# Performance work log

Measured on AMD Instinct MI355X. Metric: run time of the kernel, lower is better.

## Reference

```python
import jax, jax.numpy as jnp
import numpy as np

N = 50000
NUM_GRAPHS = 64
EPS = 1e-16  # PyG softmax denominator epsilon


def _gat_conv(x, src, dst, W, a_src, a_dst, b, heads, out_ch):
    n = x.shape[0]
    h = (x @ W).reshape(n, heads, out_ch)                    # [N,H,C]
    al_s = jnp.einsum('nhc,hc->nh', h, a_src)                # [N,H]
    al_d = jnp.einsum('nhc,hc->nh', h, a_dst)                # [N,H]
    e = jax.nn.leaky_relu(al_s[src] + al_d[dst], 0.2)        # [E,H]
    emax = jax.ops.segment_max(e, dst, num_segments=n)       # [N,H]
    ee = jnp.exp(e - emax[dst])
    den = jax.ops.segment_sum(ee, dst, num_segments=n)       # [N,H]
    alpha = ee / (den[dst] + EPS)                            # [E,H]
    msg = h[src] * alpha[:, :, None]                         # [E,H,C]
    out = jax.ops.segment_sum(msg, dst, num_segments=n)      # [N,H,C]
    return out.reshape(n, heads * out_ch) + b


def setup_inputs() -> dict:
    key = jax.random.key(0)
    ks = jax.random.split(key, 16)
    E = 250000
    x = jax.random.normal(ks[0], (N, 11), dtype=jnp.float32)
    edge_index = jax.random.randint(ks[1], (2, E), 0, N, dtype=jnp.int64)
    batch = jnp.sort(jax.random.randint(ks[2], (N,), 0, NUM_GRAPHS, dtype=jnp.int64))
    def glorot(k, shape):
        fan = shape[0] + shape[-1]
        return jax.random.uniform(k, shape, jnp.float32, -1.0, 1.0) * np.sqrt(6.0 / fan)
    return {
        'x': x, 'edge_index': edge_index, 'batch': batch,
        'W1': glorot(ks[3], (11, 8 * 128)),
        'a1s': glorot(ks[4], (8, 128)), 'a1d': glorot(ks[5], (8, 128)),
        'b1': jnp.zeros((8 * 128,), jnp.float32),
        'W2': glorot(ks[6], (1024, 8 * 64)),
        'a2s': glorot(ks[7], (8, 64)), 'a2d': glorot(ks[8], (8, 64)),
        'b2': jnp.zeros((8 * 64,), jnp.float32),
        'W3': glorot(ks[9], (512, 4 * 32)),
        'a3s': glorot(ks[10], (4, 32)), 'a3d': glorot(ks[11], (4, 32)),
        'b3': jnp.zeros((4 * 32,), jnp.float32),
        'Wout': glorot(ks[12], (128, 1)),
        'bout': jnp.zeros((1,), jnp.float32),
    }


def reference(x, edge_index, batch, W1, a1s, a1d, b1, W2, a2s, a2d, b2,
              W3, a3s, a3d, b3, Wout, bout):
    n = x.shape[0]
    # GATConv adds self-loops by default
    loop = jnp.arange(n, dtype=edge_index.dtype)
    src = jnp.concatenate([edge_index[0], loop])
    dst = jnp.concatenate([edge_index[1], loop])
    h = jax.nn.leaky_relu(_gat_conv(x, src, dst, W1, a1s, a1d, b1, 8, 128), 0.01)
    h = jax.nn.leaky_relu(_gat_conv(h, src, dst, W2, a2s, a2d, b2, 8, 64), 0.01)
    h = jax.nn.leaky_relu(_gat_conv(h, src, dst, W3, a3s, a3d, b3, 4, 32), 0.01)
    # global mean pool over graphs
    sums = jax.ops.segment_sum(h, batch, num_segments=NUM_GRAPHS)      # [G,128]
    cnt = jax.ops.segment_sum(jnp.ones((n,), h.dtype), batch, num_segments=NUM_GRAPHS)
    pooled = sums / jnp.maximum(cnt, 1.0)[:, None]
    return pooled @ Wout + bout                                        # [G,1]
```

## Files before the change

kernel.cpp:

```cpp
#include <hip/hip_runtime.h>

#define EPS 1e-16f

typedef __attribute__((ext_vector_type(8))) short short8;
typedef __attribute__((ext_vector_type(4))) float f32x4;

__device__ __forceinline__ float b2f(unsigned short u) {
    return __uint_as_float(((unsigned)u) << 16);
}
__device__ __forceinline__ unsigned short f2b(float f) {
    unsigned u = __float_as_uint(f);
    u += 0x7fffu + ((u >> 16) & 1u);
    return (unsigned short)(u >> 16);
}

typedef __attribute__((address_space(3))) void lds_vp;
typedef __attribute__((address_space(1))) const void glb_vp;
__device__ __forceinline__ void load_lds16(const unsigned short* g,
                                           unsigned short* l) {
    __builtin_amdgcn_global_load_lds((glb_vp*)g, (lds_vp*)l, 16, 0, 0);
}

__global__ void init_deg_kernel(int* deg, int N) {
    int i = blockIdx.x * blockDim.x + threadIdx.x;
    if (i < N) deg[i] = 1;
}

__global__ void hist_kernel(const int* __restrict__ ei, int E, int N, int* deg) {
    int e = blockIdx.x * blockDim.x + threadIdx.x;
    if (e < E) {
        int d = ei[E + e];
        if ((unsigned)d < (unsigned)N) atomicAdd(&deg[d], 1);
    }
}

__global__ void scan_block_kernel(const int* __restrict__ deg,
                                  int* __restrict__ rowst,
                                  int* __restrict__ bsum, int N) {
    __shared__ int s[256];
    int t = threadIdx.x, b = blockIdx.x;
    int i = b * 256 + t;
    s[t] = (i < N) ? deg[i] : 0;
    __syncthreads();
    for (int o = 1; o < 256; o <<= 1) {
        int a = (t >= o) ? s[t - o] : 0;
        __syncthreads();
        s[t] += a;
        __syncthreads();
    }
    if (i < N) rowst[i + 1] = s[t];
    if (t == 255) bsum[b] = s[255];
}

__global__ void scan_top_kernel(const int* __restrict__ bsum,
                                int* __restrict__ boff, int NB) {
    __shared__ int psum[65];
    int t = threadIdx.x;
    int chunk = (NB + 63) / 64;
    int lo = t * chunk, hi = lo + chunk;
    if (lo > NB) lo = NB;
    if (hi > NB) hi = NB;
    int s = 0;
    for (int i = lo; i < hi; i++) s += bsum[i];
    psum[t + 1] = s;
    __syncthreads();
    if (t == 0) {
        psum[0] = 0;
        for (int i = 1; i <= 64; i++) psum[i] += psum[i - 1];
    }
    __syncthreads();
    int run = psum[t];
    for (int i = lo; i < hi; i++) {
        boff[i] = run;
        run += bsum[i];
    }
}

__global__ void scan_finish_kernel(int* __restrict__ rowst,
                                   const int* __restrict__ boff,
                                   const int* __restrict__ deg,
                                   int* __restrict__ srcs,
                                   int* __restrict__ cursor, int N) {
    int i = blockIdx.x * 256 + threadIdx.x;
    if (i == 0) rowst[0] = 0;
    if (i < N) {
        int incl = rowst[i + 1] + boff[blockIdx.x];
        rowst[i + 1] = incl;
        int st = incl - deg[i];
        srcs[st] = i;
        cursor[i] = st + 1;
    }
}

__global__ void scatter_kernel(const int* __restrict__ ei, int E, int N,
                               int* cursor, int* srcs) {
    int e = blockIdx.x * blockDim.x + threadIdx.x;
    if (e < E) {
        int d = ei[E + e];
        if ((unsigned)d < (unsigned)N) {
            int p = atomicAdd(&cursor[d], 1);
            int s = ei[e];
            if ((unsigned)s >= (unsigned)N) s = d;
            srcs[p] = s;
        }
    }
}

__global__ void wprep_kernel(const float* __restrict__ W1,
                             const float* __restrict__ W2,
                             const float* __restrict__ W3,
                             unsigned short* __restrict__ wt2,
                             unsigned short* __restrict__ wt3,
                             unsigned short* __restrict__ w1sk) {
    int i = blockIdx.x * blockDim.x + threadIdx.x;
    if (i < 1024 * 512) {
        int k = i / 512, n = i % 512;
        wt2[(size_t)n * 1024 + k] = f2b(W2[i]);
    } else if (i < 1024 * 512 + 512 * 128) {
        int j = i - 1024 * 512;
        int k = j / 128, n = j % 128;
        wt3[(size_t)n * 512 + k] = f2b(W3[j]);
    } else if (i < 1024 * 512 + 512 * 128 + 8 * 128 * 32) {
        int q = i - (1024 * 512 + 512 * 128);
        int h = q >> 12, rem = q & 4095;
        int c = rem >> 5, kk = rem & 31;
        int off = (h == 7) ? 16 : 0;
        float v = 0.f;
        int k = kk - off;
        if (k >= 0 && k < 11) v = W1[k * 1024 + h * 128 + c];
        w1sk[q] = f2b(v);
    }
}

__global__ void al1_kernel(const float* __restrict__ x,
                           const float* __restrict__ W1,
                           const float* __restrict__ a1s,
                           const float* __restrict__ a1d,
                           float* __restrict__ als, float* __restrict__ ald,
                           int N) {
    __shared__ float was[128], wad[128];
    int t = threadIdx.x;
    if (t < 88) {
        int h = t / 11, k = t % 11;
        float s = 0.f, d = 0.f;
        for (int c = 0; c < 128; c++) {
            float w = W1[k * 1024 + h * 128 + c];
            s += w * a1s[h * 128 + c];
            d += w * a1d[h * 128 + c];
        }
        was[h * 16 + k] = s;
        wad[h * 16 + k] = d;
    }
    __syncthreads();
    int i = blockIdx.x * 256 + t;
    if (i >= N * 8) return;
    int n = i >> 3, h = i & 7;
    float s = 0.f, d = 0.f;
#pragma unroll
    for (int k = 0; k < 11; k++) {
        float xv = x[n * 11 + k];
        s += xv * was[h * 16 + k];
        d += xv * wad[h * 16 + k];
    }
    als[i] = s;
    ald[i] = d;
}

__global__ void aggx_kernel(const float* __restrict__ x,
                            const float* __restrict__ als,
                            const float* __restrict__ ald,
                            const int* __restrict__ rowst,
                            const int* __restrict__ srcs,
                            unsigned short* __restrict__ A2, int N) {
    int n = blockIdx.x;
    int t = threadIdx.x;
    int h = t >> 4, k = t & 15;
    int start = rowst[n], end = rowst[n + 1];
    float aldn = ald[n * 8 + h];
    float m = -1e30f;
    for (int idx = start + k; idx < end; idx += 16) {
        float v = als[srcs[idx] * 8 + h] + aldn;
        v = v > 0.f ? v : 0.2f * v;
        m = fmaxf(m, v);
    }
#pragma unroll
    for (int o = 1; o < 16; o <<= 1) m = fmaxf(m, __shfl_xor(m, o));
    float den = 0.f;
    for (int idx = start + k; idx < end; idx += 16) {
        float v = als[srcs[idx] * 8 + h] + aldn;
        v = v > 0.f ? v : 0.2f * v;
        den += expf(v - m);
    }
#pragma unroll
    for (int o = 1; o < 16; o <<= 1) den += __shfl_xor(den, o);
    float dinv = 1.0f / (den + EPS);

    float acc = 0.f;
    const int CH = 4;
    for (int idx = start; idx < end; idx += CH) {
        int mc = end - idx;
        if (mc > CH) mc = CH;
        int ss[CH];
        float lv[CH], xv[CH];
#pragma unroll
        for (int j = 0; j < CH; j++)
            if (j < mc) ss[j] = srcs[idx + j];
#pragma unroll
        for (int j = 0; j < CH; j++)
            if (j < mc) lv[j] = als[ss[j] * 8 + h];
#pragma unroll
        for (int j = 0; j < CH; j++)
            if (j < mc) xv[j] = (k < 11) ? x[ss[j] * 11 + k] : 0.f;
#pragma unroll
        for (int j = 0; j < CH; j++)
            if (j < mc) {
                float v = lv[j] + aldn;
                v = v > 0.f ? v : 0.2f * v;
                acc += expf(v - m) * dinv * xv[j];
            }
    }
    A2[(size_t)n * 128 + t] = f2b(acc);
}

template <bool EPI, int HB, int CC, bool SK>
__global__ __launch_bounds__(256) void gemm_mfma(
    const unsigned short* __restrict__ A, const unsigned short* __restrict__ Bt,
    unsigned short* __restrict__ C, const float* __restrict__ bias,
    const float* __restrict__ a_s, const float* __restrict__ a_d,
    float* __restrict__ als, float* __restrict__ ald, int H, int M, int N,
    int K, int lda) {
    int NX = gridDim.x;
    int bid = blockIdx.y * NX + blockIdx.x;
    int win = bid & (8 * NX - 1);
    int mg = bid / (8 * NX);
    int m_t = mg * 8 + (win & 7);
    int n_t = win >> 3;
    int bm = m_t * 128, bn = n_t * 128;
    if (bm >= M) return;

    union SMem {
        struct {
            unsigned short As[2][128 * 32];
            unsigned short Bs[2][128 * 32];
        } k;
        unsigned short Ct[128 * 132];
    };
    __shared__ __align__(16) SMem sm;
    auto& As = sm.k.As;
    auto& Bs = sm.k.Bs;
    auto& Ct = sm.Ct;

    int t = threadIdx.x;
    int w = t >> 6, lane = t & 63;
    int quad = lane >> 4, l16 = lane & 15;
    int wr = (w >> 1) * 64, wc = (w & 1) * 64;

    int kofs = 0;
    const unsigned short* Bb = Bt;
    if (SK) {
        kofs = n_t * 16;
        if (kofs > lda - 32) kofs = lda - 32;
        Bb = Bt + (size_t)n_t * 128 * 32;
    }

    int c0 = w * 128 + lane;
    int c1 = c0 + 64;
    int r0 = c0 >> 2, p0 = c0 & 3;
    int r1 = c1 >> 2, p1 = c1 & 3;
    int j0 = (p0 - (r0 >> 1)) & 3;
    int j1 = (p1 - (r1 >> 1)) & 3;
    int ga0 = bm + r0;
    if (ga0 >= M) ga0 = M - 1;
    int ga1 = bm + r1;
    if (ga1 >= M) ga1 = M - 1;
    const unsigned short* Ag0 = A + (size_t)ga0 * lda + kofs + j0 * 8;
    const unsigned short* Ag1 = A + (size_t)ga1 * lda + kofs + j1 * 8;
    size_t br0 = SK ? (size_t)r0 : (size_t)(bn + r0);
    size_t br1 = SK ? (size_t)r1 : (size_t)(bn + r1);
    const unsigned short* Bg0 = Bb + br0 * K + j0 * 8;
    const unsigned short* Bg1 = Bb + br1 * K + j1 * 8;

    auto stage = [&](int st, int k0) {
        load_lds16(Ag0 + k0, &As[st][(w * 128) * 8]);
        load_lds16(Ag1 + k0, &As[st][(w * 128 + 64) * 8]);
        load_lds16(Bg0 + k0, &Bs[st][(w * 128) * 8]);
        load_lds16(Bg1 + k0, &Bs[st][(w * 128 + 64) * 8]);
    };

    int aoff[4], boff4[4];
#pragma unroll
    for (int i = 0; i < 4; i++) {
        int ra = wr + i * 16 + l16;
        aoff[i] = ra * 32 + (((quad + (ra >> 1)) & 3) * 8);
        int rb = wc + i * 16 + l16;
        boff4[i] = rb * 32 + (((quad + (rb >> 1)) & 3) * 8);
    }

    f32x4 acc[4][4] = {};
    stage(0, 0);
    int st = 0;
    for (int k0 = 0; k0 < K; k0 += 32, st ^= 1) {
        __syncthreads();
        if (k0 + 32 < K) stage(st ^ 1, k0 + 32);
        short8 a[4], b[4];
#pragma unroll
        for (int mi = 0; mi < 4; mi++) a[mi] = *(const short8*)&As[st][aoff[mi]];
#pragma unroll
        for (int ni = 0; ni < 4; ni++) b[ni] = *(const short8*)&Bs[st][boff4[ni]];
#pragma unroll
        for (int mi = 0; mi < 4; mi++)
#pragma unroll
            for (int ni = 0; ni < 4; ni++)
                acc[mi][ni] = __builtin_amdgcn_mfma_f32_16x16x32_bf16(
                    a[mi], b[ni], acc[mi][ni], 0, 0, 0);
    }
    __syncthreads();

#pragma unroll
    for (int mi = 0; mi < 4; mi++) {
#pragma unroll
        for (int r = 0; r < 4; r++) {
            int rl = wr + mi * 16 + quad * 4 + r;
#pragma unroll
            for (int ni = 0; ni < 4; ni++) {
                int cl = wc + ni * 16 + l16;
                float v = acc[mi][ni][r];
                if (EPI) {
                    v += bias[bn + cl];
                    v = v > 0.f ? v : 0.01f * v;
                }
                Ct[rl * 132 + cl] = f2b(v);
            }
        }
    }
    __syncthreads();
#pragma unroll
    for (int p = 0; p < 16; p++) {
        int q = p * 256 + t;
        int row = q >> 5, c8 = q & 31;
        if (bm + row < M) {
            uint2 v = *(const uint2*)&Ct[row * 132 + c8 * 4];
            *(uint2*)&C[(size_t)(bm + row) * N + bn + c8 * 4] = v;
        }
    }
    if (HB > 0) {
        for (int pi = t; pi < 128 * HB; pi += 256) {
            int row = pi / HB, hl = pi % HB;
            if (bm + row >= M) continue;
            int hg = bn / CC + hl;
            const unsigned short* rp = &Ct[row * 132 + hl * CC];
            const float* asp = a_s + hg * CC;
            const float* adp = a_d + hg * CC;
            float s = 0.f, d = 0.f;
#pragma unroll
            for (int c = 0; c < CC; c++) {
                float v = b2f(rp[c]);
                s += v * asp[c];
                d += v * adp[c];
            }
            als[(size_t)(bm + row) * H + hg] = s;
            ald[(size_t)(bm + row) * H + hg] = d;
        }
    }
}

template <int H, int C>
__global__ void agg_fused4(const unsigned short* __restrict__ hin,
                           const float* __restrict__ als,
                           const float* __restrict__ ald,
                           const int* __restrict__ rowst,
                           const int* __restrict__ srcs,
                           const float* __restrict__ bias,
                           unsigned short* __restrict__ out, int N) {
    constexpr int HC = H * C;
    constexpr int TPH = C / 4;
    int n = blockIdx.x;
    int t = threadIdx.x;
    int c = t * 4;
    int hh = c / C;
    int li = (c % C) / 4;
    int start = rowst[n], end = rowst[n + 1];
    float aldn = ald[n * H + hh];
    float m = -1e30f;
    for (int idx = start + li; idx < end; idx += TPH) {
        float v = als[srcs[idx] * H + hh] + aldn;
        v = v > 0.f ? v : 0.2f * v;
        m = fmaxf(m, v);
    }
#pragma unroll
    for (int o = 1; o < TPH; o <<= 1) m = fmaxf(m, __shfl_xor(m, o));
    float den = 0.f;
    for (int idx = start + li; idx < end; idx += TPH) {
        float v = als[srcs[idx] * H + hh] + aldn;
        v = v > 0.f ? v : 0.2f * v;
        den += expf(v - m);
    }
#pragma unroll
    for (int o = 1; o < TPH; o <<= 1) den += __shfl_xor(den, o);
    float dinv = 1.0f / (den + EPS);

    float a0 = 0.f, a1 = 0.f, a2 = 0.f, a3 = 0.f;
    const int CH = 4;
    for (int idx = start; idx < end; idx += CH) {
        int mc = end - idx;
        if (mc > CH) mc = CH;
        int ss[CH];
        float lv[CH];
        ushort4 uv[CH];
#pragma unroll
        for (int j = 0; j < CH; j++)
            if (j < mc) ss[j] = srcs[idx + j];
#pragma unroll
        for (int j = 0; j < CH; j++)
            if (j < mc) lv[j] = als[ss[j] * H + hh];
#pragma unroll
        for (int j = 0; j < CH; j++)
            if (j < mc) uv[j] = *(const ushort4*)(hin + (size_t)ss[j] * HC + c);
#pragma unroll
        for (int j = 0; j < CH; j++)
            if (j < mc) {
                float v = lv[j] + aldn;
                v = v > 0.f ? v : 0.2f * v;
                float a = expf(v - m) * dinv;
                a0 += a * b2f(uv[j].x);
                a1 += a * b2f(uv[j].y);
                a2 += a * b2f(uv[j].z);
                a3 += a * b2f(uv[j].w);
            }
    }
    float v0 = a0 + bias[c], v1 = a1 + bias[c + 1];
    float v2 = a2 + bias[c + 2], v3 = a3 + bias[c + 3];
    ushort4 o;
    o.x = f2b(v0 > 0.f ? v0 : 0.01f * v0);
    o.y = f2b(v1 > 0.f ? v1 : 0.01f * v1);
    o.z = f2b(v2 > 0.f ? v2 : 0.01f * v2);
    o.w = f2b(v3 > 0.f ? v3 : 0.01f * v3);
    *(ushort4*)&out[(size_t)n * HC + c] = o;
}

template <int H, int C>
__global__ void agg_fused2(const unsigned short* __restrict__ hin,
                           const float* __restrict__ als,
                           const float* __restrict__ ald,
                           const int* __restrict__ rowst,
                           const int* __restrict__ srcs,
                           const float* __restrict__ bias,
                           unsigned short* __restrict__ out, int N) {
    constexpr int HC = H * C;
    constexpr int TPH = C / 2;
    int n = blockIdx.x;
    int t = threadIdx.x;
    int c = t * 2;
    int hh = c / C;
    int li = (c % C) / 2;
    int start = rowst[n], end = rowst[n + 1];
    float aldn = ald[n * H + hh];
    float m = -1e30f;
    for (int idx = start + li; idx < end; idx += TPH) {
        float v = als[srcs[idx] * H + hh] + aldn;
        v = v > 0.f ? v : 0.2f * v;
        m = fmaxf(m, v);
    }
#pragma unroll
    for (int o = 1; o < TPH; o <<= 1) m = fmaxf(m, __shfl_xor(m, o));
    float den = 0.f;
    for (int idx = start + li; idx < end; idx += TPH) {
        float v = als[srcs[idx] * H + hh] + aldn;
        v = v > 0.f ? v : 0.2f * v;
        den += expf(v - m);
    }
#pragma unroll
    for (int o = 1; o < TPH; o <<= 1) den += __shfl_xor(den, o);
    float dinv = 1.0f / (den + EPS);

    float a0 = 0.f, a1 = 0.f;
    const int CH = 4;
    for (int idx = start; idx < end; idx += CH) {
        int mc = end - idx;
        if (mc > CH) mc = CH;
        int ss[CH];
        float lv[CH];
        ushort2 uv[CH];
#pragma unroll
        for (int j = 0; j < CH; j++)
            if (j < mc) ss[j] = srcs[idx + j];
#pragma unroll
        for (int j = 0; j < CH; j++)
            if (j < mc) lv[j] = als[ss[j] * H + hh];
#pragma unroll
        for (int j = 0; j < CH; j++)
            if (j < mc) uv[j] = *(const ushort2*)(hin + (size_t)ss[j] * HC + c);
#pragma unroll
        for (int j = 0; j < CH; j++)
            if (j < mc) {
                float v = lv[j] + aldn;
                v = v > 0.f ? v : 0.2f * v;
                float a = expf(v - m) * dinv;
                a0 += a * b2f(uv[j].x);
                a1 += a * b2f(uv[j].y);
            }
    }
    float v0 = a0 + bias[c], v1 = a1 + bias[c + 1];
    ushort2 o;
    o.x = f2b(v0 > 0.f ? v0 : 0.01f * v0);
    o.y = f2b(v1 > 0.f ? v1 : 0.01f * v1);
    *(ushort2*)&out[(size_t)n * HC + c] = o;
}

__global__ void pool_init_kernel(float* pool, int GC) {
    int i = blockIdx.x * blockDim.x + threadIdx.x;
    if (i < GC) pool[i] = 0.f;
}

__global__ void pool_partial_kernel(const unsigned short* __restrict__ h3,
                                    const int* __restrict__ batch,
                                    float* __restrict__ pool, int N, int G) {
    int lo = blockIdx.x * 128;
    int hi = lo + 128;
    if (hi > N) hi = N;
    if (lo >= N) return;
    int t = threadIdx.x;
    int cur = batch[lo];
    float acc = 0.f;
    for (int n = lo; n < hi; n++) {
        int g = batch[n];
        if (g != cur) {
            if ((unsigned)cur < (unsigned)G) atomicAdd(&pool[cur * 128 + t], acc);
            acc = 0.f;
            cur = g;
        }
        acc += b2f(h3[(size_t)n * 128 + t]);
    }
    if ((unsigned)cur < (unsigned)G) atomicAdd(&pool[cur * 128 + t], acc);
}

__global__ void head_kernel(const float* __restrict__ pool,
                            const int* __restrict__ batch,
                            const float* __restrict__ Wout,
                            const float* __restrict__ bout,
                            float* __restrict__ out, int N) {
    int g = blockIdx.x;
    int t = threadIdx.x;
    int lo, hi;
    {
        int a = 0, b = N;
        while (a < b) { int mid = (a + b) >> 1; if (batch[mid] < g) a = mid + 1; else b = mid; }
        lo = a;
        a = lo; b = N;
        while (a < b) { int mid = (a + b) >> 1; if (batch[mid] < g + 1) a = mid + 1; else b = mid; }
        hi = a;
    }
    float c = (float)(hi - lo);
    c = c > 1.f ? c : 1.f;
    float v = (pool[g * 128 + t] / c) * Wout[t];
    for (int o = 32; o; o >>= 1) v += __shfl_xor(v, o);
    __shared__ float partial[2];
    if ((t & 63) == 0) partial[t >> 6] = v;
    __syncthreads();
    if (t == 0) out[g] = partial[0] + partial[1] + bout[0];
}

extern "C" void kernel_launch(void* const* d_in, const int* in_sizes, int n_in,
                              void* d_out, int out_size, void* d_ws,
                              size_t ws_size, hipStream_t stream) {
    const float* x = (const float*)d_in[0];
    const int* ei = (const int*)d_in[1];
    const int* batch = (const int*)d_in[2];
    const float* W1 = (const float*)d_in[3];
    const float* a1s = (const float*)d_in[4];
    const float* a1d = (const float*)d_in[5];
    const float* b1 = (const float*)d_in[6];
    const float* W2 = (const float*)d_in[7];
    const float* a2s = (const float*)d_in[8];
    const float* a2d = (const float*)d_in[9];
    const float* b2 = (const float*)d_in[10];
    const float* W3 = (const float*)d_in[11];
    const float* a3s = (const float*)d_in[12];
    const float* a3d = (const float*)d_in[13];
    const float* b3 = (const float*)d_in[14];
    const float* Wout = (const float*)d_in[15];
    const float* bout = (const float*)d_in[16];
    float* out = (float*)d_out;

    const int N = in_sizes[0] / 11;
    const int E = in_sizes[1] / 2;
    const int Etot = E + N;
    const int G = out_size;
    const int NB = (N + 255) / 256;
    const int MT = ((N + 127) / 128 + 7) / 8 * 8;

    char* ws = (char*)d_ws;
    size_t off = 0;
    auto alloc = [&](size_t bytes) -> void* {
        void* p = ws + off;
        off += (bytes + 255) & ~(size_t)255;
        return p;
    };
    unsigned short* buf1 = (unsigned short*)alloc((size_t)N * 1024 * 2);
    unsigned short* buf2 = (unsigned short*)alloc((size_t)N * 1024 * 2);
    float* als = (float*)alloc((size_t)N * 8 * 4);
    float* ald = (float*)alloc((size_t)N * 8 * 4);
    int* rowst = (int*)alloc((size_t)(N + 1) * 4);
    int* cursor = (int*)alloc((size_t)N * 4);
    int* srcs = (int*)alloc((size_t)Etot * 4);
    int* deg = (int*)alloc((size_t)N * 4);
    int* bsum = (int*)alloc((size_t)NB * 4);
    int* boff = (int*)alloc((size_t)NB * 4);
    float* pool = (float*)alloc((size_t)G * 128 * 4);
    unsigned short* aggx = (unsigned short*)alloc((size_t)N * 128 * 2);
    unsigned short* w1sk = (unsigned short*)alloc((size_t)8 * 128 * 32 * 2);
    unsigned short* wt2 = (unsigned short*)alloc((size_t)1024 * 512 * 2);
    unsigned short* wt3 = (unsigned short*)alloc((size_t)512 * 128 * 2);

    int nb = (N + 255) / 256;
    int eb = (E + 255) / 256;

    init_deg_kernel<<<nb, 256, 0, stream>>>(deg, N);
    hist_kernel<<<eb, 256, 0, stream>>>(ei, E, N, deg);
    scan_block_kernel<<<NB, 256, 0, stream>>>(deg, rowst, bsum, N);
    scan_top_kernel<<<1, 64, 0, stream>>>(bsum, boff, NB);
    scan_finish_kernel<<<NB, 256, 0, stream>>>(rowst, boff, deg, srcs, cursor,
                                               N);
    scatter_kernel<<<eb, 256, 0, stream>>>(ei, E, N, cursor, srcs);

    const int WTOT = 1024 * 512 + 512 * 128 + 8 * 128 * 32;
    wprep_kernel<<<(WTOT + 255) / 256, 256, 0, stream>>>(W1, W2, W3, wt2, wt3,
                                                         w1sk);

    al1_kernel<<<(N * 8 + 255) / 256, 256, 0, stream>>>(x, W1, a1s, a1d, als,
                                                        ald, N);
    aggx_kernel<<<N, 128, 0, stream>>>(x, als, ald, rowst, srcs, aggx, N);
    gemm_mfma<true, 0, 1, true><<<dim3(8, MT), 256, 0, stream>>>(
        aggx, w1sk, buf2, b1, nullptr, nullptr, nullptr, nullptr, 0, N, 1024,
        32, 128);

    gemm_mfma<false, 2, 64, false><<<dim3(4, MT), 256, 0, stream>>>(
        buf2, wt2, buf1, nullptr, a2s, a2d, als, ald, 8, N, 512, 1024, 1024);
    agg_fused4<8, 64><<<N, 128, 0, stream>>>(buf1, als, ald, rowst, srcs, b2,
                                             buf2, N);

    gemm_mfma<false, 4, 32, false><<<dim3(1, MT), 256, 0, stream>>>(
        buf2, wt3, buf1, nullptr, a3s, a3d, als, ald, 4, N, 128, 512, 512);
    agg_fused2<4, 32><<<N, 64, 0, stream>>>(buf1, als, ald, rowst, srcs, b3,
                                            buf2, N);

    pool_init_kernel<<<(G * 128 + 255) / 256, 256, 0, stream>>>(pool, G * 128);
    pool_partial_kernel<<<(N + 127) / 128, 128, 0, stream>>>(buf2, batch, pool,
                                                             N, G);
    head_kernel<<<G, 128, 0, stream>>>(pool, batch, Wout, bout, out, N);
}
```

Measured before the change: 512.3 us.

## Precompute layer-1 attention coefficients per edge in a separate softmax kernel

Splits the layer-1 attention softmax out of the aggregation kernel. A new per-(node,head) kernel computes the max, denominator and normalized alpha, and stores them per edge in a scratch buffer. The aggregation then only multiplies alpha by x. W1·a1 is also precomputed once in a single-block kernel instead of inside every al1 block. This removes the redundant exp and gather work repeated across the 16 lanes per head, at the cost of an extra launch and an Etot*8 float scratch array that is written and then read back.

```diff
diff --git a/kernel.cpp b/kernel.cpp
--- a/kernel.cpp
+++ b/kernel.cpp
@@ -132,43 +132,104 @@
     }
 }
 
-__global__ void al1_kernel(const float* __restrict__ x,
-                           const float* __restrict__ W1,
+__global__ void wa1_kernel(const float* __restrict__ W1,
                            const float* __restrict__ a1s,
                            const float* __restrict__ a1d,
+                           float* __restrict__ w_as, float* __restrict__ w_ad) {
+    int t = threadIdx.x;
+    if (t >= 88) return;
+    int h = t / 11, k = t % 11;
+    float s = 0.f, d = 0.f;
+    for (int c = 0; c < 128; c++) {
+        float w = W1[k * 1024 + h * 128 + c];
+        s += w * a1s[h * 128 + c];
+        d += w * a1d[h * 128 + c];
+    }
+    w_as[h * 16 + k] = s;
+    w_ad[h * 16 + k] = d;
+}
+
+__global__ void al1_kernel(const float* __restrict__ x,
+                           const float* __restrict__ w_as,
+                           const float* __restrict__ w_ad,
                            float* __restrict__ als, float* __restrict__ ald,
                            int N) {
-    __shared__ float was[128], wad[128];
-    int t = threadIdx.x;
-    if (t < 88) {
-        int h = t / 11, k = t % 11;
-        float s = 0.f, d = 0.f;
-        for (int c = 0; c < 128; c++) {
-            float w = W1[k * 1024 + h * 128 + c];
-            s += w * a1s[h * 128 + c];
-            d += w * a1d[h * 128 + c];
-        }
-        was[h * 16 + k] = s;
-        wad[h * 16 + k] = d;
-    }
-    __syncthreads();
-    int i = blockIdx.x * 256 + t;
+    int i = blockIdx.x * blockDim.x + threadIdx.x;
     if (i >= N * 8) return;
     int n = i >> 3, h = i & 7;
     float s = 0.f, d = 0.f;
 #pragma unroll
     for (int k = 0; k < 11; k++) {
         float xv = x[n * 11 + k];
-        s += xv * was[h * 16 + k];
-        d += xv * wad[h * 16 + k];
+        s += xv * w_as[h * 16 + k];
+        d += xv * w_ad[h * 16 + k];
     }
     als[i] = s;
     ald[i] = d;
 }
 
+template <int H>
+__global__ void mden_kernel(const float* __restrict__ als,
+                            const float* __restrict__ ald,
+                            const int* __restrict__ rowst,
+                            const int* __restrict__ srcs,
+                            float* __restrict__ escr, int N) {
+    int i = blockIdx.x * blockDim.x + threadIdx.x;
+    if (i >= N * H) return;
+    int n = i / H, h = i % H;
+    float aldn = ald[i];
+    int start = rowst[n], end = rowst[n + 1];
+    const int CH = 4;
+    float m = -1e30f;
+    for (int idx = start; idx < end; idx += CH) {
+        int mc = end - idx;
+        if (mc > CH) mc = CH;
+        int ss[CH];
+        float lv[CH];
+#pragma unroll
+        for (int j = 0; j < CH; j++)
+            if (j < mc) ss[j] = srcs[idx + j];
+#pragma unroll
+        for (int j = 0; j < CH; j++)
+            if (j < mc) lv[j] = als[ss[j] * H + h];
+#pragma unroll
+        for (int j = 0; j < CH; j++)
+            if (j < mc) {
+                float v = lv[j] + aldn;
+                v = v > 0.f ? v : 0.2f * v;
+                escr[(size_t)(idx + j) * H + h] = v;
+                m = fmaxf(m, v);
+            }
+    }
+    float den = 0.f;
+    for (int idx = start; idx < end; idx += CH) {
+        int mc = end - idx;
+        if (mc > CH) mc = CH;
+        float lv[CH];
+#pragma unroll
+        for (int j = 0; j < CH; j++)
+            if (j < mc) lv[j] = escr[(size_t)(idx + j) * H + h];
+#pragma unroll
+        for (int j = 0; j < CH; j++)
+            if (j < mc) den += expf(lv[j] - m);
+    }
+    float dinv = 1.0f / (den + EPS);
+    for (int idx = start; idx < end; idx += CH) {
+        int mc = end - idx;
+        if (mc > CH) mc = CH;
+        float lv[CH];
+#pragma unroll
+        for (int j = 0; j < CH; j++)
+            if (j < mc) lv[j] = escr[(size_t)(idx + j) * H + h];
+#pragma unroll
+        for (int j = 0; j < CH; j++)
+            if (j < mc)
+                escr[(size_t)(idx + j) * H + h] = expf(lv[j] - m) * dinv;
+    }
+}
+
 __global__ void aggx_kernel(const float* __restrict__ x,
-                            const float* __restrict__ als,
-                            const float* __restrict__ ald,
+                            const float* __restrict__ escr,
                             const int* __restrict__ rowst,
                             const int* __restrict__ srcs,
                             unsigned short* __restrict__ A2, int N) {
@@ -176,48 +237,25 @@
     int t = threadIdx.x;
     int h = t >> 4, k = t & 15;
     int start = rowst[n], end = rowst[n + 1];
-    float aldn = ald[n * 8 + h];
-    float m = -1e30f;
-    for (int idx = start + k; idx < end; idx += 16) {
-        float v = als[srcs[idx] * 8 + h] + aldn;
-        v = v > 0.f ? v : 0.2f * v;
-        m = fmaxf(m, v);
-    }
-#pragma unroll
-    for (int o = 1; o < 16; o <<= 1) m = fmaxf(m, __shfl_xor(m, o));
-    float den = 0.f;
-    for (int idx = start + k; idx < end; idx += 16) {
-        float v = als[srcs[idx] * 8 + h] + aldn;
-        v = v > 0.f ? v : 0.2f * v;
-        den += expf(v - m);
-    }
-#pragma unroll
-    for (int o = 1; o < 16; o <<= 1) den += __shfl_xor(den, o);
-    float dinv = 1.0f / (den + EPS);
-
     float acc = 0.f;
     const int CH = 4;
     for (int idx = start; idx < end; idx += CH) {
         int mc = end - idx;
         if (mc > CH) mc = CH;
         int ss[CH];
-        float lv[CH], xv[CH];
+        float av[CH], xv[CH];
 #pragma unroll
         for (int j = 0; j < CH; j++)
             if (j < mc) ss[j] = srcs[idx + j];
 #pragma unroll
         for (int j = 0; j < CH; j++)
-            if (j < mc) lv[j] = als[ss[j] * 8 + h];
+            if (j < mc) av[j] = escr[(size_t)(idx + j) * 8 + h];
 #pragma unroll
         for (int j = 0; j < CH; j++)
             if (j < mc) xv[j] = (k < 11) ? x[ss[j] * 11 + k] : 0.f;
 #pragma unroll
         for (int j = 0; j < CH; j++)
-            if (j < mc) {
-                float v = lv[j] + aldn;
-                v = v > 0.f ? v : 0.2f * v;
-                acc += expf(v - m) * dinv * xv[j];
-            }
+            if (j < mc) acc += av[j] * xv[j];
     }
     A2[(size_t)n * 128 + t] = f2b(acc);
 }
@@ -600,6 +638,7 @@
     unsigned short* buf2 = (unsigned short*)alloc((size_t)N * 1024 * 2);
     float* als = (float*)alloc((size_t)N * 8 * 4);
     float* ald = (float*)alloc((size_t)N * 8 * 4);
+    float* escr = (float*)alloc((size_t)Etot * 8 * 4);
     int* rowst = (int*)alloc((size_t)(N + 1) * 4);
     int* cursor = (int*)alloc((size_t)N * 4);
     int* srcs = (int*)alloc((size_t)Etot * 4);
@@ -611,6 +650,8 @@
     unsigned short* w1sk = (unsigned short*)alloc((size_t)8 * 128 * 32 * 2);
     unsigned short* wt2 = (unsigned short*)alloc((size_t)1024 * 512 * 2);
     unsigned short* wt3 = (unsigned short*)alloc((size_t)512 * 128 * 2);
+    float* w_as = (float*)alloc(8 * 16 * 4);
+    float* w_ad = (float*)alloc(8 * 16 * 4);
 
     int nb = (N + 255) / 256;
     int eb = (E + 255) / 256;
@@ -626,10 +667,13 @@
     const int WTOT = 1024 * 512 + 512 * 128 + 8 * 128 * 32;
     wprep_kernel<<<(WTOT + 255) / 256, 256, 0, stream>>>(W1, W2, W3, wt2, wt3,
                                                          w1sk);
-
-    al1_kernel<<<(N * 8 + 255) / 256, 256, 0, stream>>>(x, W1, a1s, a1d, als,
-                                                        ald, N);
-    aggx_kernel<<<N, 128, 0, stream>>>(x, als, ald, rowst, srcs, aggx, N);
+    wa1_kernel<<<1, 128, 0, stream>>>(W1, a1s, a1d, w_as, w_ad);
+
+    al1_kernel<<<(N * 8 + 255) / 256, 256, 0, stream>>>(x, w_as, w_ad, als, ald,
+                                                        N);
+    mden_kernel<8><<<(N * 8 + 255) / 256, 256, 0, stream>>>(als, ald, rowst,
+                                                            srcs, escr, N);
+    aggx_kernel<<<N, 128, 0, stream>>>(x, escr, rowst, srcs, aggx, N);
     gemm_mfma<true, 0, 1, true><<<dim3(8, MT), 256, 0, stream>>>(
         aggx, w1sk, buf2, b1, nullptr, nullptr, nullptr, nullptr, 0, N, 1024,
         32, 128);
```

New measurement: 483.9 us. 5.6% less time.
